# Kernel optimization log

Hardware: AMD Instinct MI355X
Metric: run time of the kernel (lower is better)

## Reference

```python
import jax, jax.numpy as jnp
import numpy as np

LN_EPS = 1e-5


def setup_inputs() -> dict:
    key = jax.random.key(0)
    ks = jax.random.split(key, 6)
    B, S, D = 4, 4096, 2048
    Db = D // 4  # bottleneck_dim = n_embd // compression_ratio
    hidden = jax.random.normal(ks[0], (B, S, D), dtype=jnp.float32)
    # LayerNorm params (torch defaults: gamma=1, beta=0)
    ln_gamma = jnp.ones((D,), dtype=jnp.float32)
    ln_beta = jnp.zeros((D,), dtype=jnp.float32)
    # Linear weights, torch default init: U(-1/sqrt(fan_in), 1/sqrt(fan_in))
    bd_lim = 1.0 / np.sqrt(D)
    W_down = jax.random.uniform(ks[1], (D, Db), minval=-bd_lim, maxval=bd_lim, dtype=jnp.float32)
    b_down = jax.random.uniform(ks[2], (Db,), minval=-bd_lim, maxval=bd_lim, dtype=jnp.float32)
    bu_lim = 1.0 / np.sqrt(Db)
    W_up = jax.random.uniform(ks[3], (Db, D), minval=-bu_lim, maxval=bu_lim, dtype=jnp.float32)
    b_up = jax.random.uniform(ks[4], (D,), minval=-bu_lim, maxval=bu_lim, dtype=jnp.float32)
    alpha = jnp.array(0.01, dtype=jnp.float32)
    return {
        "hidden": hidden,
        "ln_gamma": ln_gamma,
        "ln_beta": ln_beta,
        "W_down": W_down,
        "b_down": b_down,
        "W_up": W_up,
        "b_up": b_up,
        "alpha": alpha,
        "layer_idx": 0,
    }


def reference(hidden, ln_gamma, ln_beta, W_down, b_down, W_up, b_up, alpha, layer_idx):
    # LayerNorm over last dim
    mu = jnp.mean(hidden, axis=-1, keepdims=True)
    var = jnp.mean(jnp.square(hidden - mu), axis=-1, keepdims=True)
    h_norm = (hidden - mu) * jax.lax.rsqrt(var + LN_EPS) * ln_gamma + ln_beta
    # down-proj -> SiLU -> up-proj   [b s d] @ [d k] -> [b s k] -> [b s d]
    z = jnp.einsum("bsd,dk->bsk", h_norm, W_down) + b_down
    z = jax.nn.silu(z)
    bottleneck_out = jnp.einsum("bsk,kd->bsd", z, W_up) + b_up
    # alpha-gated residual
    return hidden + alpha * (bottleneck_out - hidden)
```

## Files before the change

### kernel.cpp

```cpp
#include <hip/hip_runtime.h>

typedef __bf16 bf16x8 __attribute__((ext_vector_type(8)));
typedef float f32x4 __attribute__((ext_vector_type(4)));

__global__ void wt_transpose_kernel(const float* __restrict__ W,
                                    __bf16* __restrict__ Wt, int K, int N) {
    int n = blockIdx.x;
    for (int k = threadIdx.x; k < K; k += blockDim.x) {
        Wt[(size_t)n * K + k] = (__bf16)W[(size_t)k * N + n];
    }
}

__global__ __launch_bounds__(256) void ln_kernel(const float* __restrict__ x,
                                                 const float* __restrict__ g,
                                                 const float* __restrict__ be,
                                                 __bf16* __restrict__ y, int D) {
    const int t = threadIdx.x;
    const size_t row = blockIdx.x;
    const float4* xr = (const float4*)(x + row * (size_t)D);
    const int nv = D >> 3;
    float s = 0.f, ss = 0.f;
    for (int i = t; i < nv; i += 256) {
        float4 v0 = xr[i * 2], v1 = xr[i * 2 + 1];
        s += v0.x + v0.y + v0.z + v0.w + v1.x + v1.y + v1.z + v1.w;
        ss += v0.x * v0.x + v0.y * v0.y + v0.z * v0.z + v0.w * v0.w +
              v1.x * v1.x + v1.y * v1.y + v1.z * v1.z + v1.w * v1.w;
    }
    for (int o = 32; o > 0; o >>= 1) {
        s += __shfl_down(s, o);
        ss += __shfl_down(ss, o);
    }
    __shared__ float ps[4], pss[4], mv[2];
    int w = t >> 6;
    if ((t & 63) == 0) { ps[w] = s; pss[w] = ss; }
    __syncthreads();
    if (t == 0) {
        float S = ps[0] + ps[1] + ps[2] + ps[3];
        float SS = pss[0] + pss[1] + pss[2] + pss[3];
        float mu = S / (float)D;
        float var = SS / (float)D - mu * mu;
        mv[0] = mu;
        mv[1] = rsqrtf(var + 1e-5f);
    }
    __syncthreads();
    float mu = mv[0], rstd = mv[1];
    const float4* gg = (const float4*)g;
    const float4* bb = (const float4*)be;
    bf16x8* yr = (bf16x8*)(y + row * (size_t)D);
    for (int i = t; i < nv; i += 256) {
        float4 v0 = xr[i * 2], v1 = xr[i * 2 + 1];
        float4 g0 = gg[i * 2], g1 = gg[i * 2 + 1];
        float4 b0 = bb[i * 2], b1 = bb[i * 2 + 1];
        bf16x8 o;
        o[0] = (__bf16)((v0.x - mu) * rstd * g0.x + b0.x);
        o[1] = (__bf16)((v0.y - mu) * rstd * g0.y + b0.y);
        o[2] = (__bf16)((v0.z - mu) * rstd * g0.z + b0.z);
        o[3] = (__bf16)((v0.w - mu) * rstd * g0.w + b0.w);
        o[4] = (__bf16)((v1.x - mu) * rstd * g1.x + b1.x);
        o[5] = (__bf16)((v1.y - mu) * rstd * g1.y + b1.y);
        o[6] = (__bf16)((v1.z - mu) * rstd * g1.z + b1.z);
        o[7] = (__bf16)((v1.w - mu) * rstd * g1.w + b1.w);
        yr[i] = o;
    }
}

template <int EPI>
__global__ __launch_bounds__(256) void gemm_bt(const __bf16* __restrict__ A,
                                               const __bf16* __restrict__ Bt,
                                               const float* __restrict__ bias,
                                               const float* __restrict__ hid,
                                               const float* __restrict__ alpha_p,
                                               void* __restrict__ Cout,
                                               int M, int N, int K) {
    constexpr int BM = 128, BN = 128, BK = 32;
    __shared__ __align__(16) __bf16 Ads[BM * BK];
    __shared__ __align__(16) __bf16 Bds[BN * BK];

    const int tid = threadIdx.x;
    const int wave = tid >> 6;
    const int lane = tid & 63;
    const int bn = blockIdx.x, bm = blockIdx.y;
    const int row0 = bm * BM, col0 = bn * BN;
    const int wr = wave >> 1, wc = wave & 1;

    f32x4 acc[4][4] = {};

    const __bf16* Ag = A + (size_t)row0 * K;
    const __bf16* Bg = Bt + (size_t)col0 * K;
    const int lrow = lane >> 2;
    const int lk = (lane & 3) * 8;

    const int c = lane & 15;
    const int q = lane >> 4;

    for (int k0 = 0; k0 < K; k0 += BK) {
#pragma unroll
        for (int p = 0; p < 2; ++p) {
            int r = wave * 32 + p * 16;
            __builtin_amdgcn_global_load_lds(
                (__attribute__((address_space(1))) void*)(Ag + (size_t)(r + lrow) * K + k0 + lk),
                (__attribute__((address_space(3))) void*)(Ads + r * BK),
                16, 0, 0);
            __builtin_amdgcn_global_load_lds(
                (__attribute__((address_space(1))) void*)(Bg + (size_t)(r + lrow) * K + k0 + lk),
                (__attribute__((address_space(3))) void*)(Bds + r * BK),
                16, 0, 0);
        }
        __syncthreads();

        bf16x8 af[4], bfr[4];
#pragma unroll
        for (int i = 0; i < 4; ++i)
            af[i] = *(const bf16x8*)(Ads + (wr * 64 + i * 16 + c) * BK + q * 8);
#pragma unroll
        for (int j = 0; j < 4; ++j)
            bfr[j] = *(const bf16x8*)(Bds + (wc * 64 + j * 16 + c) * BK + q * 8);
#pragma unroll
        for (int i = 0; i < 4; ++i)
#pragma unroll
            for (int j = 0; j < 4; ++j)
                acc[i][j] = __builtin_amdgcn_mfma_f32_16x16x32_bf16(af[i], bfr[j],
                                                                    acc[i][j], 0, 0, 0);
        __syncthreads();
    }

    float alpha = (EPI == 1) ? *alpha_p : 0.f;
#pragma unroll
    for (int i = 0; i < 4; ++i) {
#pragma unroll
        for (int j = 0; j < 4; ++j) {
            int colg = col0 + wc * 64 + j * 16 + c;
            float bv = bias[colg];
#pragma unroll
            for (int r = 0; r < 4; ++r) {
                int rowg = row0 + wr * 64 + i * 16 + q * 4 + r;
                size_t idx = (size_t)rowg * N + colg;
                float v = acc[i][j][r] + bv;
                if (EPI == 0) {
                    float sv = v / (1.f + __expf(-v));
                    ((__bf16*)Cout)[idx] = (__bf16)sv;
                } else {
                    float h = hid[idx];
                    ((float*)Cout)[idx] = h + alpha * (v - h);
                }
            }
        }
    }
}

extern "C" void kernel_launch(void* const* d_in, const int* in_sizes, int n_in,
                              void* d_out, int out_size, void* d_ws, size_t ws_size,
                              hipStream_t stream) {
    const float* hidden = (const float*)d_in[0];
    const float* ln_gamma = (const float*)d_in[1];
    const float* ln_beta = (const float*)d_in[2];
    const float* W_down = (const float*)d_in[3];
    const float* b_down = (const float*)d_in[4];
    const float* W_up = (const float*)d_in[5];
    const float* b_up = (const float*)d_in[6];
    const float* alpha = (const float*)d_in[7];
    float* out = (float*)d_out;

    const int D = in_sizes[2];
    const int Db = in_sizes[4];
    const int M = in_sizes[0] / D;

    char* w = (char*)d_ws;
    __bf16* hn = (__bf16*)w;   w += (size_t)M * D * sizeof(__bf16);
    __bf16* z = (__bf16*)w;    w += (size_t)M * Db * sizeof(__bf16);
    __bf16* Wtd = (__bf16*)w;  w += (size_t)D * Db * sizeof(__bf16);
    __bf16* Wtu = (__bf16*)w;  w += (size_t)Db * D * sizeof(__bf16);

    wt_transpose_kernel<<<Db, 256, 0, stream>>>(W_down, Wtd, D, Db);
    wt_transpose_kernel<<<D, 256, 0, stream>>>(W_up, Wtu, Db, D);

    ln_kernel<<<M, 256, 0, stream>>>(hidden, ln_gamma, ln_beta, hn, D);

    gemm_bt<0><<<dim3(Db / 128, M / 128), 256, 0, stream>>>(
        hn, Wtd, b_down, nullptr, nullptr, (void*)z, M, Db, D);

    gemm_bt<1><<<dim3(D / 128, M / 128), 256, 0, stream>>>(
        z, Wtu, b_up, hidden, alpha, (void*)out, M, D, Db);
}
```

Baseline: 412.7 us.

## Tile weight transpose through LDS and vectorize GEMM epilogue via swapped MFMA operands

Replaces the two strided per-column weight transpose kernels with one merged launch that transposes 32x32 tiles through padded shared memory, so global reads and writes are coalesced. Swaps the MFMA A/B operands so each lane's four accumulator values lie along consecutive output columns. The epilogue can then use float4 bias and hidden loads and vector stores instead of scalar strided accesses. This targets uncoalesced memory traffic in the transpose and in the output epilogue.

```diff
diff --git a/kernel.cpp b/kernel.cpp
--- a/kernel.cpp
+++ b/kernel.cpp
@@ -1,14 +1,34 @@
 #include <hip/hip_runtime.h>
 
 typedef __bf16 bf16x8 __attribute__((ext_vector_type(8)));
+typedef __bf16 bf16x4 __attribute__((ext_vector_type(4)));
 typedef float f32x4 __attribute__((ext_vector_type(4)));
 
-__global__ void wt_transpose_kernel(const float* __restrict__ W,
-                                    __bf16* __restrict__ Wt, int K, int N) {
-    int n = blockIdx.x;
-    for (int k = threadIdx.x; k < K; k += blockDim.x) {
-        Wt[(size_t)n * K + k] = (__bf16)W[(size_t)k * N + n];
-    }
+__global__ __launch_bounds__(256) void prep_kernel(const float* __restrict__ Wd,
+                                                   __bf16* __restrict__ Wtd,
+                                                   const float* __restrict__ Wu,
+                                                   __bf16* __restrict__ Wtu,
+                                                   int D, int Db) {
+    const float* W;
+    __bf16* Wt;
+    int K, N, tile;
+    const int ntile_d = (Db / 32) * (D / 32);
+    if ((int)blockIdx.x < ntile_d) {
+        W = Wd; Wt = Wtd; K = D; N = Db; tile = blockIdx.x;
+    } else {
+        W = Wu; Wt = Wtu; K = Db; N = D; tile = blockIdx.x - ntile_d;
+    }
+    const int tn = tile % (N / 32), tk = tile / (N / 32);
+    const int n0 = tn * 32, k0 = tk * 32;
+    __shared__ float t[32][33];
+    const int c = threadIdx.x & 31, r0 = threadIdx.x >> 5;
+#pragma unroll
+    for (int r = r0; r < 32; r += 8)
+        t[r][c] = W[(size_t)(k0 + r) * N + n0 + c];
+    __syncthreads();
+#pragma unroll
+    for (int r = r0; r < 32; r += 8)
+        Wt[(size_t)(n0 + r) * K + k0 + c] = (__bf16)t[c][r];
 }
 
 __global__ __launch_bounds__(256) void ln_kernel(const float* __restrict__ x,
@@ -108,18 +128,18 @@
         }
         __syncthreads();
 
-        bf16x8 af[4], bfr[4];
+        bf16x8 afW[4], bfA[4];
+#pragma unroll
+        for (int j = 0; j < 4; ++j)
+            afW[j] = *(const bf16x8*)(Bds + (wc * 64 + j * 16 + c) * BK + q * 8);
 #pragma unroll
         for (int i = 0; i < 4; ++i)
-            af[i] = *(const bf16x8*)(Ads + (wr * 64 + i * 16 + c) * BK + q * 8);
-#pragma unroll
-        for (int j = 0; j < 4; ++j)
-            bfr[j] = *(const bf16x8*)(Bds + (wc * 64 + j * 16 + c) * BK + q * 8);
+            bfA[i] = *(const bf16x8*)(Ads + (wr * 64 + i * 16 + c) * BK + q * 8);
 #pragma unroll
         for (int i = 0; i < 4; ++i)
 #pragma unroll
             for (int j = 0; j < 4; ++j)
-                acc[i][j] = __builtin_amdgcn_mfma_f32_16x16x32_bf16(af[i], bfr[j],
+                acc[i][j] = __builtin_amdgcn_mfma_f32_16x16x32_bf16(afW[j], bfA[i],
                                                                     acc[i][j], 0, 0, 0);
         __syncthreads();
     }
@@ -127,22 +147,31 @@
     float alpha = (EPI == 1) ? *alpha_p : 0.f;
 #pragma unroll
     for (int i = 0; i < 4; ++i) {
+        const int rowg = row0 + wr * 64 + i * 16 + c;
 #pragma unroll
         for (int j = 0; j < 4; ++j) {
-            int colg = col0 + wc * 64 + j * 16 + c;
-            float bv = bias[colg];
-#pragma unroll
-            for (int r = 0; r < 4; ++r) {
-                int rowg = row0 + wr * 64 + i * 16 + q * 4 + r;
-                size_t idx = (size_t)rowg * N + colg;
-                float v = acc[i][j][r] + bv;
-                if (EPI == 0) {
-                    float sv = v / (1.f + __expf(-v));
-                    ((__bf16*)Cout)[idx] = (__bf16)sv;
-                } else {
-                    float h = hid[idx];
-                    ((float*)Cout)[idx] = h + alpha * (v - h);
-                }
+            const int colb = col0 + wc * 64 + j * 16 + q * 4;
+            const float4 bv = *(const float4*)(bias + colb);
+            float v0 = acc[i][j][0] + bv.x;
+            float v1 = acc[i][j][1] + bv.y;
+            float v2 = acc[i][j][2] + bv.z;
+            float v3 = acc[i][j][3] + bv.w;
+            const size_t idx = (size_t)rowg * N + colb;
+            if (EPI == 0) {
+                bf16x4 o;
+                o[0] = (__bf16)(v0 / (1.f + __expf(-v0)));
+                o[1] = (__bf16)(v1 / (1.f + __expf(-v1)));
+                o[2] = (__bf16)(v2 / (1.f + __expf(-v2)));
+                o[3] = (__bf16)(v3 / (1.f + __expf(-v3)));
+                *(bf16x4*)((__bf16*)Cout + idx) = o;
+            } else {
+                const float4 h = *(const float4*)(hid + idx);
+                float4 o;
+                o.x = h.x + alpha * (v0 - h.x);
+                o.y = h.y + alpha * (v1 - h.y);
+                o.z = h.z + alpha * (v2 - h.z);
+                o.w = h.w + alpha * (v3 - h.w);
+                *(float4*)((float*)Cout + idx) = o;
             }
         }
     }
@@ -166,13 +195,13 @@
     const int M = in_sizes[0] / D;
 
     char* w = (char*)d_ws;
-    __bf16* hn = (__bf16*)w;   w += (size_t)M * D * sizeof(__bf16);
-    __bf16* z = (__bf16*)w;    w += (size_t)M * Db * sizeof(__bf16);
-    __bf16* Wtd = (__bf16*)w;  w += (size_t)D * Db * sizeof(__bf16);
-    __bf16* Wtu = (__bf16*)w;  w += (size_t)Db * D * sizeof(__bf16);
-
-    wt_transpose_kernel<<<Db, 256, 0, stream>>>(W_down, Wtd, D, Db);
-    wt_transpose_kernel<<<D, 256, 0, stream>>>(W_up, Wtu, Db, D);
+    __bf16* hn = (__bf16*)w;  w += (size_t)M * D * sizeof(__bf16);
+    __bf16* z = (__bf16*)w;   w += (size_t)M * Db * sizeof(__bf16);
+    __bf16* Wtd = (__bf16*)w; w += (size_t)D * Db * sizeof(__bf16);
+    __bf16* Wtu = (__bf16*)w; w += (size_t)Db * D * sizeof(__bf16);
+
+    const int ntiles = 2 * (D / 32) * (Db / 32);
+    prep_kernel<<<ntiles, 256, 0, stream>>>(W_down, Wtd, W_up, Wtu, D, Db);
 
     ln_kernel<<<M, 256, 0, stream>>>(hidden, ln_gamma, ln_beta, hn, D);
 
```

After: 395.3 us. 1.04x faster.
